# Kernel tuning notes

Hardware: AMD Instinct MI355X
Metric: run time of the kernel (lower is better)

## Reference

```python
import jax, jax.numpy as jnp
import numpy as np

MAX_Z = 54  # atomic numbers up to iodine (53)
_mv = np.full(MAX_Z, 4.0, np.float32)
for z, v in {6: 4, 7: 3, 8: 2, 16: 6, 9: 1, 17: 1, 35: 1, 53: 1, 15: 5, 1: 1}.items():
    _mv[z] = v
_vdw = np.full(MAX_Z, 1.6, np.float32)  # default_radius = 1.6
for z, r in {1: 1.2, 6: 1.7, 7: 1.55, 8: 1.52, 9: 1.47, 15: 1.8, 16: 1.8, 17: 1.75, 35: 1.85, 53: 1.98}.items():
    _vdw[z] = r
_bl = np.full((MAX_Z, MAX_Z), 1.5, np.float32)  # default_length = 1.5
for (a, b), L in {(6, 6): 1.54, (6, 7): 1.47, (6, 8): 1.43, (6, 16): 1.82, (6, 9): 1.35, (6, 17): 1.77, (6, 1): 1.09, (7, 7): 1.45, (7, 8): 1.40, (7, 1): 1.01, (8, 8): 1.48, (8, 1): 0.96, (16, 16): 2.05, (15, 8): 1.63}.items():
    _bl[a, b] = L
    _bl[b, a] = L  # symmetric == tuple(sorted(...)) lookup
MAX_VAL = jnp.asarray(_mv)
VDW = jnp.asarray(_vdw)
BOND = jnp.asarray(_bl)
BIG = 1e9  # stands in for torch's float('inf') diagonal mask


def _forward(pos, edge_index, atom_types):
    N = pos.shape[0]
    row, col = edge_index[0], edge_index[1]
    # --- valence violations: scatter-add out-degree per atom ---
    bond_counts = jnp.zeros((N,), pos.dtype).at[row].add(1.0)
    violation = jnp.maximum(bond_counts - MAX_VAL[atom_types], 0.0)  # >0 iff counts > max_val
    loss = jnp.sum(violation ** 2)
    # Sequential valence push. Original loops atoms in ascending order and each atom's
    # neighbors in edge-list order; a stable sort of edges by row reproduces exactly that
    # visitation order, so a scan over sorted edges matches the sequential semantics
    # (pos_new[i] updates feed later direction computations).
    order = jnp.argsort(row)  # jnp.argsort is stable
    rs, cs = row[order], col[order]

    def step(p, rc):
        r, c = rc
        v = violation[r]
        d = p[r] - p[c]
        dist = jnp.linalg.norm(d) + 1e-8
        return p.at[r].add(jnp.where(v > 0, d / dist * v * 1e-3, 0.0)), None

    pos_new, _ = jax.lax.scan(step, pos, (rs, cs))
    # --- bond-length correction (gather per edge, scatter back per atom) ---
    bond_vec = pos_new[row] - pos_new[col]                        # [E,3]
    cur_len = jnp.linalg.norm(bond_vec, axis=-1, keepdims=True)   # [E,1]
    tgt_len = BOND[atom_types[row], atom_types[col]][:, None]     # [E,1]
    loss = loss + jnp.mean(jnp.abs(cur_len - tgt_len) ** 2)
    ratio = jnp.clip(tgt_len / (cur_len + 1e-8), 0.98, 1.02)
    adj = (bond_vec * ratio - bond_vec) * 0.01
    pos_new = pos_new + jnp.zeros_like(pos).at[row].add(adj * 0.5).at[col].add(-adj * 0.5)
    # --- steric clash repulsion over all atom pairs (cdist) ---
    sq = jnp.sum(pos_new ** 2, axis=-1)
    d2 = sq[:, None] + sq[None, :] - 2.0 * (pos_new @ pos_new.T)  # [N,N]
    eye = jnp.eye(N, dtype=bool)
    dist = jnp.sqrt(jnp.maximum(jnp.where(eye, 1.0, d2), 1e-20))
    dist = jnp.where(eye, BIG, dist)  # diagonal masked to +inf in the original
    rad = VDW[atom_types]
    min_d = (rad[:, None] + rad[None, :]) * 0.8
    loss = loss + jnp.sum(jax.nn.relu(min_d - dist) ** 2) / 2.0
    # original loops unordered clash pairs i<j updating i and j symmetrically; the full
    # symmetric double sum below is mathematically identical and avoids an [N,N,3] tensor:
    mask = (dist < min_d) & (dist > 1e-8)
    coeff = jnp.where(mask, (min_d - dist) * 0.005 * 0.5 / dist, 0.0)  # [N,N]
    steric = coeff.sum(axis=1)[:, None] * pos_new - coeff @ pos_new    # sum_j c_ij (p_i - p_j)
    return pos_new + steric, loss * 0.1


def setup_inputs() -> dict:
    key = jax.random.key(0)
    k1, k2, k3, k4 = jax.random.split(key, 4)
    N, E = 8192, 32768
    pos = jax.random.normal(k1, (N, 3), jnp.float32) * 6.0  # coords in an ~Angstrom-scale blob
    elements = jnp.array([1, 6, 7, 8, 9, 15, 16, 17], jnp.int32)  # H C N O F P S Cl
    atom_types = elements[jax.random.randint(k2, (N,), 0, 8)]
    edge_index = jnp.stack([jax.random.randint(k3, (E,), 0, N),
                            jax.random.randint(k4, (E,), 0, N)]).astype(jnp.int32)
    return {"pos": pos, "edge_index": edge_index, "atom_types": atom_types}


def reference(pos, edge_index, atom_types):
    return _forward(pos, edge_index, atom_types)
```

## Files before the change

kernel.cpp:

```cpp
#include <hip/hip_runtime.h>
#include <math.h>

#define NA 8192
#define NE 32768
#define NT 256
#define JSPLIT 32
#define JCHUNK (NA / JSPLIT)
#define NIBLK  32

#define WS_DEG      0
#define WS_LOSS     (WS_DEG + NA)
#define WS_DA       (WS_LOSS + 4)
#define WS_DC       (WS_DA + 3*NA)
#define WS_ZERO_END (WS_DC + 3*NA)
#define WS_PART     WS_ZERO_END

__device__ __forceinline__ float maxval_of(int z) {
    switch (z) {
        case 1: return 1.f; case 6: return 4.f; case 7: return 3.f; case 8: return 2.f;
        case 9: return 1.f; case 15: return 5.f; case 16: return 6.f; case 17: return 1.f;
        case 35: return 1.f; case 53: return 1.f; default: return 4.f;
    }
}
__device__ __forceinline__ float vdw_of(int z) {
    switch (z) {
        case 1: return 1.2f; case 6: return 1.7f; case 7: return 1.55f; case 8: return 1.52f;
        case 9: return 1.47f; case 15: return 1.8f; case 16: return 1.8f; case 17: return 1.75f;
        case 35: return 1.85f; case 53: return 1.98f; default: return 1.6f;
    }
}
__device__ __forceinline__ float bond_of(int a, int b) {
    int lo = a < b ? a : b, hi = a < b ? b : a;
    switch (lo * 64 + hi) {
        case 6*64+6:   return 1.54f;
        case 6*64+7:   return 1.47f;
        case 6*64+8:   return 1.43f;
        case 6*64+16:  return 1.82f;
        case 6*64+9:   return 1.35f;
        case 6*64+17:  return 1.77f;
        case 1*64+6:   return 1.09f;
        case 7*64+7:   return 1.45f;
        case 7*64+8:   return 1.40f;
        case 1*64+7:   return 1.01f;
        case 8*64+8:   return 1.48f;
        case 1*64+8:   return 0.96f;
        case 16*64+16: return 2.05f;
        case 8*64+15:  return 1.63f;
        default:       return 1.5f;
    }
}
__device__ __forceinline__ float viol_of(int d, int z) {
    return fmaxf((float)d - maxval_of(z), 0.f);
}

__device__ __forceinline__ float wave_reduce_sum(float x) {
    #pragma unroll
    for (int off = 32; off > 0; off >>= 1) x += __shfl_down(x, off);
    return x;
}

__global__ void k_degbond(const int* __restrict__ row, const int* __restrict__ col,
                          const int* __restrict__ types, const float* __restrict__ pos,
                          int* __restrict__ deg, float* __restrict__ dC,
                          float* __restrict__ lossAcc) {
    int e = blockIdx.x * NT + threadIdx.x;
    float l1 = 0.f;
    if (e < NE) {
        int r = row[e], c = col[e];
        atomicAdd(&deg[r], 1);
        float bx = pos[3*r]   - pos[3*c];
        float by = pos[3*r+1] - pos[3*c+1];
        float bz = pos[3*r+2] - pos[3*c+2];
        float cur = sqrtf(bx*bx + by*by + bz*bz);
        float tgt = bond_of(types[r], types[c]);
        float diff = cur - tgt;
        l1 = diff * diff;
        float ratio = tgt / (cur + 1e-8f);
        ratio = fminf(fmaxf(ratio, 0.98f), 1.02f);
        float s = (ratio - 1.f) * 0.01f * 0.5f;
        atomicAdd(&dC[3*r],   bx * s);
        atomicAdd(&dC[3*r+1], by * s);
        atomicAdd(&dC[3*r+2], bz * s);
        atomicAdd(&dC[3*c],   -bx * s);
        atomicAdd(&dC[3*c+1], -by * s);
        atomicAdd(&dC[3*c+2], -bz * s);
    }
    float p1 = wave_reduce_sum(l1);
    if ((threadIdx.x & 63) == 0 && p1 != 0.f) atomicAdd(&lossAcc[1], p1);
}

__global__ void k_push(const int* __restrict__ row, const int* __restrict__ col,
                       const int* __restrict__ types, const int* __restrict__ deg,
                       const float* __restrict__ pos, float* __restrict__ dA,
                       float* __restrict__ lossAcc) {
    int e = blockIdx.x * NT + threadIdx.x;
    if (e < NE) {
        int r = row[e];
        float v = viol_of(deg[r], types[r]);
        int c = col[e];
        if (v > 0.f && c != r) {
            float dx = pos[3*r]   - pos[3*c];
            float dy = pos[3*r+1] - pos[3*c+1];
            float dz = pos[3*r+2] - pos[3*c+2];
            float dist = sqrtf(dx*dx + dy*dy + dz*dz) + 1e-8f;
            float sc = v * 1e-3f / dist;
            atomicAdd(&dA[3*r],   dx * sc);
            atomicAdd(&dA[3*r+1], dy * sc);
            atomicAdd(&dA[3*r+2], dz * sc);
        }
    }
    float l0 = 0.f;
    if (e < NA) {
        float v = viol_of(deg[e], types[e]);
        l0 = v * v;
    }
    float p0 = wave_reduce_sum(l0);
    if ((threadIdx.x & 63) == 0 && p0 != 0.f) atomicAdd(&lossAcc[0], p0);
}

__device__ __forceinline__ void steric_pair(const float4 p, const float4 q,
                                            float& cs, float& sx, float& sy, float& sz,
                                            float& ll) {
    float dx = p.x - q.x, dy = p.y - q.y, dz = p.z - q.z;
    float d2 = fmaf(dx, dx, fmaf(dy, dy, dz * dz));
    float md = p.w + q.w;
    float rinv = rsqrtf(fmaxf(d2, 1e-12f));
    float dist = d2 * rinv;
    float t1 = md - dist;
    bool ok = (t1 > 0.f) && (d2 > 1e-12f);
    float t1c = ok ? t1 : 0.f;
    ll = fmaf(t1c, t1c, ll);
    float co = t1c * rinv;
    cs += co;
    sx = fmaf(co, q.x, sx);
    sy = fmaf(co, q.y, sy);
    sz = fmaf(co, q.z, sz);
}

__global__ void __launch_bounds__(NT)
k_steric(const float* __restrict__ pos, const float* __restrict__ dA,
         const float* __restrict__ dC, const int* __restrict__ types,
         float4* __restrict__ partial, float* __restrict__ lossAcc) {
    __shared__ float4 sm[JCHUNK];
    const int t = threadIdx.x;
    const int b = blockIdx.x;
    const int yb = b >> 5;
    const int ib = b & 31;
    int j = yb * JCHUNK + t;
    sm[t] = make_float4(pos[3*j]   + dA[3*j]   + dC[3*j],
                        pos[3*j+1] + dA[3*j+1] + dC[3*j+1],
                        pos[3*j+2] + dA[3*j+2] + dC[3*j+2],
                        vdw_of(types[j]) * 0.8f);
    int i = ib * NT + t;
    float4 p = make_float4(pos[3*i]   + dA[3*i]   + dC[3*i],
                           pos[3*i+1] + dA[3*i+1] + dC[3*i+1],
                           pos[3*i+2] + dA[3*i+2] + dC[3*i+2],
                           vdw_of(types[i]) * 0.8f);
    __syncthreads();
    float cs = 0.f, sx = 0.f, sy = 0.f, sz = 0.f, ll = 0.f;
    #pragma unroll 8
    for (int jj = 0; jj < JCHUNK; jj++) {
        steric_pair(p, sm[jj], cs, sx, sy, sz, ll);
    }
    partial[yb * NA + i] = make_float4(cs, sx, sy, sz);
    float part = wave_reduce_sum(ll);
    if ((t & 63) == 0 && part != 0.f) atomicAdd(&lossAcc[2], part);
}

__global__ void k_reduce(const float* __restrict__ pos, const float* __restrict__ dA,
                         const float* __restrict__ dC, const float4* __restrict__ partial,
                         const float* __restrict__ lossAcc, float* __restrict__ out) {
    int a = blockIdx.x * NT + threadIdx.x;
    float cs = 0.f, sx = 0.f, sy = 0.f, sz = 0.f;
    #pragma unroll 8
    for (int y = 0; y < JSPLIT; y++) {
        float4 u = partial[y * NA + a];
        cs += u.x; sx += u.y; sy += u.z; sz += u.w;
    }
    float px = pos[3*a]   + dA[3*a]   + dC[3*a];
    float py = pos[3*a+1] + dA[3*a+1] + dC[3*a+1];
    float pz = pos[3*a+2] + dA[3*a+2] + dC[3*a+2];
    float c = 1.f + cs * 0.0025f;
    out[3*a]   = px * c - sx * 0.0025f;
    out[3*a+1] = py * c - sy * 0.0025f;
    out[3*a+2] = pz * c - sz * 0.0025f;
    if (a == 0) {
        float loss = lossAcc[0] + lossAcc[1] * (1.f / NE) + lossAcc[2] * 0.5f;
        out[3*NA] = loss * 0.1f;
    }
}

extern "C" void kernel_launch(void* const* d_in, const int* in_sizes, int n_in,
                              void* d_out, int out_size, void* d_ws, size_t ws_size,
                              hipStream_t stream) {
    (void)in_sizes; (void)n_in; (void)out_size; (void)ws_size;
    const float* pos   = (const float*)d_in[0];
    const int*   eidx  = (const int*)d_in[1];
    const int*   types = (const int*)d_in[2];
    const int* row = eidx;
    const int* col = eidx + NE;

    int*   ws_i = (int*)d_ws;
    float* ws_f = (float*)d_ws;
    int*    deg     = ws_i + WS_DEG;
    float*  lossAcc = ws_f + WS_LOSS;
    float*  dA      = ws_f + WS_DA;
    float*  dC      = ws_f + WS_DC;
    float4* partial = (float4*)(ws_f + WS_PART);
    float*  out     = (float*)d_out;

    hipMemsetAsync(d_ws, 0, (size_t)WS_ZERO_END * 4, stream);
    k_degbond<<<NE/NT, NT, 0, stream>>>(row, col, types, pos, deg, dC, lossAcc);
    k_push   <<<NE/NT, NT, 0, stream>>>(row, col, types, deg, pos, dA, lossAcc);
    k_steric <<<JSPLIT*NIBLK, NT, 0, stream>>>(pos, dA, dC, types, partial, lossAcc);
    k_reduce <<<NA/NT, NT, 0, stream>>>(pos, dA, dC, partial, lossAcc, out);
}
```

Measured before the change: 153.3 us.

## Fuse final reduction into steric kernel via last-block counters, 2 atoms per thread

The separate reduce kernel is removed. Each steric block now increments a per-i-tile counter, and the last block for that tile sums the JSPLIT partials and writes the output. A global counter lets the final block write the loss. Each thread now handles two i atoms, so every shared-memory j load is reused twice, which halves the block count. Zeroing of dA and of the counters moves into the earlier kernels to shrink the memset. The cost is threadfence and atomic overhead, and a serialized tail in which only 16 blocks do the reduction.

Result: slower. 167.1 us (+9.0%).

```diff
diff --git a/kernel.cpp b/kernel.cpp
--- a/kernel.cpp
+++ b/kernel.cpp
@@ -6,14 +6,18 @@
 #define NT 256
 #define JSPLIT 32
 #define JCHUNK (NA / JSPLIT)
-#define NIBLK  32
+#define NIB 16
+#define NBLK (JSPLIT * NIB)
 
 #define WS_DEG      0
 #define WS_LOSS     (WS_DEG + NA)
-#define WS_DA       (WS_LOSS + 4)
-#define WS_DC       (WS_DA + 3*NA)
-#define WS_ZERO_END (WS_DC + 3*NA)
-#define WS_PART     WS_ZERO_END
+#define WS_DC       (WS_LOSS + 4)
+#define WS_MEMSET_END (WS_DC + 3*NA)
+#define WS_CNT      WS_MEMSET_END
+#define WS_GCNT     (WS_CNT + NIB)
+#define WS_DA       (WS_GCNT + 1)
+#define WS_PART_RAW (WS_DA + 3*NA)
+#define WS_PART     ((WS_PART_RAW + 3) & ~3)
 
 __device__ __forceinline__ float maxval_of(int z) {
     switch (z) {
@@ -62,8 +66,9 @@
 __global__ void k_degbond(const int* __restrict__ row, const int* __restrict__ col,
                           const int* __restrict__ types, const float* __restrict__ pos,
                           int* __restrict__ deg, float* __restrict__ dC,
-                          float* __restrict__ lossAcc) {
+                          float* __restrict__ dA, float* __restrict__ lossAcc) {
     int e = blockIdx.x * NT + threadIdx.x;
+    if (e < 3 * NA) dA[e] = 0.f;
     float l1 = 0.f;
     if (e < NE) {
         int r = row[e], c = col[e];
@@ -92,8 +97,9 @@
 __global__ void k_push(const int* __restrict__ row, const int* __restrict__ col,
                        const int* __restrict__ types, const int* __restrict__ deg,
                        const float* __restrict__ pos, float* __restrict__ dA,
-                       float* __restrict__ lossAcc) {
+                       int* __restrict__ cnt, float* __restrict__ lossAcc) {
     int e = blockIdx.x * NT + threadIdx.x;
+    if (e < NIB + 1) cnt[e] = 0;
     if (e < NE) {
         int r = row[e];
         float v = viol_of(deg[r], types[r]);
@@ -140,53 +146,81 @@
 __global__ void __launch_bounds__(NT)
 k_steric(const float* __restrict__ pos, const float* __restrict__ dA,
          const float* __restrict__ dC, const int* __restrict__ types,
-         float4* __restrict__ partial, float* __restrict__ lossAcc) {
+         float4* __restrict__ partial, float* __restrict__ lossAcc,
+         int* __restrict__ cnt, float* __restrict__ out) {
     __shared__ float4 sm[JCHUNK];
+    __shared__ int sLast, sGlob;
     const int t = threadIdx.x;
     const int b = blockIdx.x;
-    const int yb = b >> 5;
-    const int ib = b & 31;
+    const int yb = b >> 4;
+    const int ib = b & 15;
     int j = yb * JCHUNK + t;
     sm[t] = make_float4(pos[3*j]   + dA[3*j]   + dC[3*j],
                         pos[3*j+1] + dA[3*j+1] + dC[3*j+1],
                         pos[3*j+2] + dA[3*j+2] + dC[3*j+2],
                         vdw_of(types[j]) * 0.8f);
-    int i = ib * NT + t;
-    float4 p = make_float4(pos[3*i]   + dA[3*i]   + dC[3*i],
-                           pos[3*i+1] + dA[3*i+1] + dC[3*i+1],
-                           pos[3*i+2] + dA[3*i+2] + dC[3*i+2],
-                           vdw_of(types[i]) * 0.8f);
+    const int i0 = ib * 512 + t;
+    const int i1 = i0 + 256;
+    float4 p0 = make_float4(pos[3*i0]   + dA[3*i0]   + dC[3*i0],
+                            pos[3*i0+1] + dA[3*i0+1] + dC[3*i0+1],
+                            pos[3*i0+2] + dA[3*i0+2] + dC[3*i0+2],
+                            vdw_of(types[i0]) * 0.8f);
+    float4 p1 = make_float4(pos[3*i1]   + dA[3*i1]   + dC[3*i1],
+                            pos[3*i1+1] + dA[3*i1+1] + dC[3*i1+1],
+                            pos[3*i1+2] + dA[3*i1+2] + dC[3*i1+2],
+                            vdw_of(types[i1]) * 0.8f);
     __syncthreads();
-    float cs = 0.f, sx = 0.f, sy = 0.f, sz = 0.f, ll = 0.f;
-    #pragma unroll 8
-    for (int jj = 0; jj < JCHUNK; jj++) {
-        steric_pair(p, sm[jj], cs, sx, sy, sz, ll);
-    }
-    partial[yb * NA + i] = make_float4(cs, sx, sy, sz);
+    float cs0 = 0.f, sx0 = 0.f, sy0 = 0.f, sz0 = 0.f;
+    float cs1 = 0.f, sx1 = 0.f, sy1 = 0.f, sz1 = 0.f;
+    float ll = 0.f;
+    #pragma unroll 2
+    for (int jj = 0; jj < JCHUNK; jj += 4) {
+        float4 q0 = sm[jj], q1 = sm[jj+1], q2 = sm[jj+2], q3 = sm[jj+3];
+        steric_pair(p0, q0, cs0, sx0, sy0, sz0, ll);
+        steric_pair(p1, q0, cs1, sx1, sy1, sz1, ll);
+        steric_pair(p0, q1, cs0, sx0, sy0, sz0, ll);
+        steric_pair(p1, q1, cs1, sx1, sy1, sz1, ll);
+        steric_pair(p0, q2, cs0, sx0, sy0, sz0, ll);
+        steric_pair(p1, q2, cs1, sx1, sy1, sz1, ll);
+        steric_pair(p0, q3, cs0, sx0, sy0, sz0, ll);
+        steric_pair(p1, q3, cs1, sx1, sy1, sz1, ll);
+    }
+    partial[yb * NA + i0] = make_float4(cs0, sx0, sy0, sz0);
+    partial[yb * NA + i1] = make_float4(cs1, sx1, sy1, sz1);
     float part = wave_reduce_sum(ll);
     if ((t & 63) == 0 && part != 0.f) atomicAdd(&lossAcc[2], part);
-}
-
-__global__ void k_reduce(const float* __restrict__ pos, const float* __restrict__ dA,
-                         const float* __restrict__ dC, const float4* __restrict__ partial,
-                         const float* __restrict__ lossAcc, float* __restrict__ out) {
-    int a = blockIdx.x * NT + threadIdx.x;
-    float cs = 0.f, sx = 0.f, sy = 0.f, sz = 0.f;
-    #pragma unroll 8
-    for (int y = 0; y < JSPLIT; y++) {
-        float4 u = partial[y * NA + a];
-        cs += u.x; sx += u.y; sy += u.z; sz += u.w;
-    }
-    float px = pos[3*a]   + dA[3*a]   + dC[3*a];
-    float py = pos[3*a+1] + dA[3*a+1] + dC[3*a+1];
-    float pz = pos[3*a+2] + dA[3*a+2] + dC[3*a+2];
-    float c = 1.f + cs * 0.0025f;
-    out[3*a]   = px * c - sx * 0.0025f;
-    out[3*a+1] = py * c - sy * 0.0025f;
-    out[3*a+2] = pz * c - sz * 0.0025f;
-    if (a == 0) {
+
+    __threadfence();
+    __syncthreads();
+    if (t == 0) {
+        int r1 = __hip_atomic_fetch_add(&cnt[ib], 1, __ATOMIC_ACQ_REL, __HIP_MEMORY_SCOPE_AGENT);
+        sLast = (r1 == JSPLIT - 1);
+        int r2 = __hip_atomic_fetch_add(&cnt[NIB], 1, __ATOMIC_ACQ_REL, __HIP_MEMORY_SCOPE_AGENT);
+        sGlob = (r2 == NBLK - 1);
+    }
+    __syncthreads();
+    if (sGlob && t == 0) {
         float loss = lossAcc[0] + lossAcc[1] * (1.f / NE) + lossAcc[2] * 0.5f;
         out[3*NA] = loss * 0.1f;
+    }
+    if (sLast) {
+        #pragma unroll
+        for (int k = 0; k < 2; k++) {
+            int a = ib * 512 + k * 256 + t;
+            float cs = 0.f, sx = 0.f, sy = 0.f, sz = 0.f;
+            #pragma unroll 8
+            for (int y = 0; y < JSPLIT; y++) {
+                float4 u = partial[y * NA + a];
+                cs += u.x; sx += u.y; sy += u.z; sz += u.w;
+            }
+            float px = pos[3*a]   + dA[3*a]   + dC[3*a];
+            float py = pos[3*a+1] + dA[3*a+1] + dC[3*a+1];
+            float pz = pos[3*a+2] + dA[3*a+2] + dC[3*a+2];
+            float c = 1.f + cs * 0.0025f;
+            out[3*a]   = px * c - sx * 0.0025f;
+            out[3*a+1] = py * c - sy * 0.0025f;
+            out[3*a+2] = pz * c - sz * 0.0025f;
+        }
     }
 }
 
@@ -204,14 +238,14 @@
     float* ws_f = (float*)d_ws;
     int*    deg     = ws_i + WS_DEG;
     float*  lossAcc = ws_f + WS_LOSS;
+    float*  dC      = ws_f + WS_DC;
+    int*    cnt     = ws_i + WS_CNT;
     float*  dA      = ws_f + WS_DA;
-    float*  dC      = ws_f + WS_DC;
     float4* partial = (float4*)(ws_f + WS_PART);
     float*  out     = (float*)d_out;
 
-    hipMemsetAsync(d_ws, 0, (size_t)WS_ZERO_END * 4, stream);
-    k_degbond<<<NE/NT, NT, 0, stream>>>(row, col, types, pos, deg, dC, lossAcc);
-    k_push   <<<NE/NT, NT, 0, stream>>>(row, col, types, deg, pos, dA, lossAcc);
-    k_steric <<<JSPLIT*NIBLK, NT, 0, stream>>>(pos, dA, dC, types, partial, lossAcc);
-    k_reduce <<<NA/NT, NT, 0, stream>>>(pos, dA, dC, partial, lossAcc, out);
-}
+    hipMemsetAsync(d_ws, 0, (size_t)WS_MEMSET_END * 4, stream);
+    k_degbond<<<NE/NT, NT, 0, stream>>>(row, col, types, pos, deg, dC, dA, lossAcc);
+    k_push   <<<NE/NT, NT, 0, stream>>>(row, col, types, deg, pos, dA, cnt, lossAcc);
+    k_steric <<<NBLK,  NT, 0, stream>>>(pos, dA, dC, types, partial, lossAcc, cnt, out);
+}
```

## Process two atoms per thread in steric kernel and merge displacement buffers

Applied to the files above, without the earlier changes.

Each steric thread now accumulates two i-atoms against every shared-memory j entry, so each LDS load is reused twice and there is more ILP. The j-split becomes runtime-selectable (64 chunks of 128 when workspace allows, else 32). The push and bond-correction displacements now go into a single buffer, which removes extra loads and memset bytes. Costs are more registers per thread and, at jsplit 64, twice the partial-sum traffic in the reduce kernel.

Result: no change. 154.2 us (+0.6%).

```diff
diff --git a/kernel.cpp b/kernel.cpp
--- a/kernel.cpp
+++ b/kernel.cpp
@@ -4,16 +4,13 @@
 #define NA 8192
 #define NE 32768
 #define NT 256
-#define JSPLIT 32
-#define JCHUNK (NA / JSPLIT)
-#define NIBLK  32
+#define NIB 16
 
 #define WS_DEG      0
 #define WS_LOSS     (WS_DEG + NA)
-#define WS_DA       (WS_LOSS + 4)
-#define WS_DC       (WS_DA + 3*NA)
-#define WS_ZERO_END (WS_DC + 3*NA)
-#define WS_PART     WS_ZERO_END
+#define WS_DD       (WS_LOSS + 4)
+#define WS_ZERO_END (WS_DD + 3*NA)
+#define WS_PART     ((WS_ZERO_END + 3) & ~3)
 
 __device__ __forceinline__ float maxval_of(int z) {
     switch (z) {
@@ -61,7 +58,7 @@
 
 __global__ void k_degbond(const int* __restrict__ row, const int* __restrict__ col,
                           const int* __restrict__ types, const float* __restrict__ pos,
-                          int* __restrict__ deg, float* __restrict__ dC,
+                          int* __restrict__ deg, float* __restrict__ dD,
                           float* __restrict__ lossAcc) {
     int e = blockIdx.x * NT + threadIdx.x;
     float l1 = 0.f;
@@ -78,12 +75,12 @@
         float ratio = tgt / (cur + 1e-8f);
         ratio = fminf(fmaxf(ratio, 0.98f), 1.02f);
         float s = (ratio - 1.f) * 0.01f * 0.5f;
-        atomicAdd(&dC[3*r],   bx * s);
-        atomicAdd(&dC[3*r+1], by * s);
-        atomicAdd(&dC[3*r+2], bz * s);
-        atomicAdd(&dC[3*c],   -bx * s);
-        atomicAdd(&dC[3*c+1], -by * s);
-        atomicAdd(&dC[3*c+2], -bz * s);
+        atomicAdd(&dD[3*r],   bx * s);
+        atomicAdd(&dD[3*r+1], by * s);
+        atomicAdd(&dD[3*r+2], bz * s);
+        atomicAdd(&dD[3*c],   -bx * s);
+        atomicAdd(&dD[3*c+1], -by * s);
+        atomicAdd(&dD[3*c+2], -bz * s);
     }
     float p1 = wave_reduce_sum(l1);
     if ((threadIdx.x & 63) == 0 && p1 != 0.f) atomicAdd(&lossAcc[1], p1);
@@ -91,7 +88,7 @@
 
 __global__ void k_push(const int* __restrict__ row, const int* __restrict__ col,
                        const int* __restrict__ types, const int* __restrict__ deg,
-                       const float* __restrict__ pos, float* __restrict__ dA,
+                       const float* __restrict__ pos, float* __restrict__ dD,
                        float* __restrict__ lossAcc) {
     int e = blockIdx.x * NT + threadIdx.x;
     if (e < NE) {
@@ -104,9 +101,9 @@
             float dz = pos[3*r+2] - pos[3*c+2];
             float dist = sqrtf(dx*dx + dy*dy + dz*dz) + 1e-8f;
             float sc = v * 1e-3f / dist;
-            atomicAdd(&dA[3*r],   dx * sc);
-            atomicAdd(&dA[3*r+1], dy * sc);
-            atomicAdd(&dA[3*r+2], dz * sc);
+            atomicAdd(&dD[3*r],   dx * sc);
+            atomicAdd(&dD[3*r+1], dy * sc);
+            atomicAdd(&dD[3*r+2], dz * sc);
         }
     }
     float l0 = 0.f;
@@ -138,48 +135,56 @@
 }
 
 __global__ void __launch_bounds__(NT)
-k_steric(const float* __restrict__ pos, const float* __restrict__ dA,
-         const float* __restrict__ dC, const int* __restrict__ types,
-         float4* __restrict__ partial, float* __restrict__ lossAcc) {
-    __shared__ float4 sm[JCHUNK];
+k_steric(const float* __restrict__ pos, const float* __restrict__ dD,
+         const int* __restrict__ types, float4* __restrict__ partial,
+         float* __restrict__ lossAcc, int jchunk) {
+    __shared__ float4 sm[256];
     const int t = threadIdx.x;
-    const int b = blockIdx.x;
-    const int yb = b >> 5;
-    const int ib = b & 31;
-    int j = yb * JCHUNK + t;
-    sm[t] = make_float4(pos[3*j]   + dA[3*j]   + dC[3*j],
-                        pos[3*j+1] + dA[3*j+1] + dC[3*j+1],
-                        pos[3*j+2] + dA[3*j+2] + dC[3*j+2],
-                        vdw_of(types[j]) * 0.8f);
-    int i = ib * NT + t;
-    float4 p = make_float4(pos[3*i]   + dA[3*i]   + dC[3*i],
-                           pos[3*i+1] + dA[3*i+1] + dC[3*i+1],
-                           pos[3*i+2] + dA[3*i+2] + dC[3*i+2],
-                           vdw_of(types[i]) * 0.8f);
+    const int yb = blockIdx.x >> 4;
+    const int ib = blockIdx.x & 15;
+    if (t < jchunk) {
+        int j = yb * jchunk + t;
+        sm[t] = make_float4(pos[3*j]   + dD[3*j],
+                            pos[3*j+1] + dD[3*j+1],
+                            pos[3*j+2] + dD[3*j+2],
+                            vdw_of(types[j]) * 0.8f);
+    }
+    const int i0 = ib * 512 + t;
+    const int i1 = i0 + 256;
+    float4 p0 = make_float4(pos[3*i0] + dD[3*i0], pos[3*i0+1] + dD[3*i0+1],
+                            pos[3*i0+2] + dD[3*i0+2], vdw_of(types[i0]) * 0.8f);
+    float4 p1 = make_float4(pos[3*i1] + dD[3*i1], pos[3*i1+1] + dD[3*i1+1],
+                            pos[3*i1+2] + dD[3*i1+2], vdw_of(types[i1]) * 0.8f);
     __syncthreads();
-    float cs = 0.f, sx = 0.f, sy = 0.f, sz = 0.f, ll = 0.f;
+    float cs0 = 0.f, sx0 = 0.f, sy0 = 0.f, sz0 = 0.f;
+    float cs1 = 0.f, sx1 = 0.f, sy1 = 0.f, sz1 = 0.f;
+    float ll = 0.f;
     #pragma unroll 8
-    for (int jj = 0; jj < JCHUNK; jj++) {
-        steric_pair(p, sm[jj], cs, sx, sy, sz, ll);
-    }
-    partial[yb * NA + i] = make_float4(cs, sx, sy, sz);
+    for (int jj = 0; jj < jchunk; jj++) {
+        float4 q = sm[jj];
+        steric_pair(p0, q, cs0, sx0, sy0, sz0, ll);
+        steric_pair(p1, q, cs1, sx1, sy1, sz1, ll);
+    }
+    partial[yb * NA + i0] = make_float4(cs0, sx0, sy0, sz0);
+    partial[yb * NA + i1] = make_float4(cs1, sx1, sy1, sz1);
     float part = wave_reduce_sum(ll);
     if ((t & 63) == 0 && part != 0.f) atomicAdd(&lossAcc[2], part);
 }
 
-__global__ void k_reduce(const float* __restrict__ pos, const float* __restrict__ dA,
-                         const float* __restrict__ dC, const float4* __restrict__ partial,
-                         const float* __restrict__ lossAcc, float* __restrict__ out) {
+__global__ void k_reduce(const float* __restrict__ pos, const float* __restrict__ dD,
+                         const float4* __restrict__ partial,
+                         const float* __restrict__ lossAcc, float* __restrict__ out,
+                         int jsplit) {
     int a = blockIdx.x * NT + threadIdx.x;
     float cs = 0.f, sx = 0.f, sy = 0.f, sz = 0.f;
     #pragma unroll 8
-    for (int y = 0; y < JSPLIT; y++) {
+    for (int y = 0; y < jsplit; y++) {
         float4 u = partial[y * NA + a];
         cs += u.x; sx += u.y; sy += u.z; sz += u.w;
     }
-    float px = pos[3*a]   + dA[3*a]   + dC[3*a];
-    float py = pos[3*a+1] + dA[3*a+1] + dC[3*a+1];
-    float pz = pos[3*a+2] + dA[3*a+2] + dC[3*a+2];
+    float px = pos[3*a]   + dD[3*a];
+    float py = pos[3*a+1] + dD[3*a+1];
+    float pz = pos[3*a+2] + dD[3*a+2];
     float c = 1.f + cs * 0.0025f;
     out[3*a]   = px * c - sx * 0.0025f;
     out[3*a+1] = py * c - sy * 0.0025f;
@@ -193,7 +198,7 @@
 extern "C" void kernel_launch(void* const* d_in, const int* in_sizes, int n_in,
                               void* d_out, int out_size, void* d_ws, size_t ws_size,
                               hipStream_t stream) {
-    (void)in_sizes; (void)n_in; (void)out_size; (void)ws_size;
+    (void)in_sizes; (void)n_in; (void)out_size;
     const float* pos   = (const float*)d_in[0];
     const int*   eidx  = (const int*)d_in[1];
     const int*   types = (const int*)d_in[2];
@@ -204,14 +209,17 @@
     float* ws_f = (float*)d_ws;
     int*    deg     = ws_i + WS_DEG;
     float*  lossAcc = ws_f + WS_LOSS;
-    float*  dA      = ws_f + WS_DA;
-    float*  dC      = ws_f + WS_DC;
+    float*  dD      = ws_f + WS_DD;
     float4* partial = (float4*)(ws_f + WS_PART);
     float*  out     = (float*)d_out;
 
+    size_t need64 = ((size_t)WS_PART + (size_t)4 * 64 * NA) * 4;
+    int jsplit = (ws_size >= need64) ? 64 : 32;
+    int jchunk = NA / jsplit;
+
     hipMemsetAsync(d_ws, 0, (size_t)WS_ZERO_END * 4, stream);
-    k_degbond<<<NE/NT, NT, 0, stream>>>(row, col, types, pos, deg, dC, lossAcc);
-    k_push   <<<NE/NT, NT, 0, stream>>>(row, col, types, deg, pos, dA, lossAcc);
-    k_steric <<<JSPLIT*NIBLK, NT, 0, stream>>>(pos, dA, dC, types, partial, lossAcc);
-    k_reduce <<<NA/NT, NT, 0, stream>>>(pos, dA, dC, partial, lossAcc, out);
-}
+    k_degbond<<<NE/NT, NT, 0, stream>>>(row, col, types, pos, deg, dD, lossAcc);
+    k_push   <<<NE/NT, NT, 0, stream>>>(row, col, types, deg, pos, dD, lossAcc);
+    k_steric <<<jsplit*NIB, NT, 0, stream>>>(pos, dD, types, partial, lossAcc, jchunk);
+    k_reduce <<<NA/NT, NT, 0, stream>>>(pos, dD, partial, lossAcc, out, jsplit);
+}
```
